# Performance work log

Hardware: AMD Instinct MI355X
Metric: run time of the kernel (lower is better)

Reference implementation:

```python
import jax, jax.numpy as jnp
import numpy as np

# --- constants from config ---
CU, CV, F, BASE = 257.446, 197.718, 387.777, 0.239965
INLIER_THRESHOLD = 0.5
ERROR_TOLERANCE = 0.5   # '3D'
NUM_ITERATIONS = 256
DIM = '3D'
BATCH, NPTS, NSAMP = 64, 16384, 6


def se3_inv(T):
    # T: ...x4x4 SE(3); inverse = [R^T, -R^T t]
    R = T[..., :3, :3]
    t = T[..., :3, 3:4]
    Rt = jnp.swapaxes(R, -1, -2)
    top = jnp.concatenate([Rt, -Rt @ t], axis=-1)
    bottom = jnp.broadcast_to(jnp.array([0.0, 0.0, 0.0, 1.0], T.dtype), top.shape[:-2] + (1, 4))
    return jnp.concatenate([top, bottom], axis=-2)


def weighted_svd_transform(src, trg, w):
    # src, trg: Bx4xS homogeneous points; w: Bx1xS weights. Returns T_trg_src (Bx4x4).
    ps, pt = src[:, :3, :], trg[:, :3, :]
    w_sum = jnp.sum(w, axis=2, keepdims=True)
    cs = jnp.sum(ps * w, axis=2, keepdims=True) / w_sum  # Bx3x1
    ct = jnp.sum(pt * w, axis=2, keepdims=True) / w_sum
    qs, qt = ps - cs, pt - ct
    cov = jnp.einsum('bis,bjs->bij', qt * w, qs)  # Bx3x3
    U, _, Vt = jnp.linalg.svd(cov)
    det = jnp.linalg.det(U @ Vt)
    diag = jnp.stack([jnp.ones_like(det), jnp.ones_like(det), det], axis=-1)  # Bx3
    R = jnp.einsum('bij,bj,bjk->bik', U, diag, Vt)
    t = ct - R @ cs
    top = jnp.concatenate([R, t], axis=2)
    bottom = jnp.broadcast_to(jnp.array([0.0, 0.0, 0.0, 1.0], src.dtype), (src.shape[0], 1, 4))
    return jnp.concatenate([top, bottom], axis=1)


def stereo_project(pts):
    # pts: Bx4xN homogeneous camera-frame points -> Bx4xN stereo image coords (ul, vl, ur, vr)
    M = jnp.array([[F, 0.0, CU, 0.0],
                   [0.0, F, CV, 0.0],
                   [F, 0.0, CU, -F * BASE],
                   [0.0, F, CV, 0.0]], pts.dtype)
    z = pts[:, 2:3, :]
    return jnp.einsum('ij,bjn->bin', M, pts) / z


def setup_inputs() -> dict:
    key = jax.random.key(0)
    ks = jax.random.split(key, 6)
    def homog(k):
        p = jax.random.normal(k, (BATCH, 3, NPTS), jnp.float32) * 5.0
        p = p.at[:, 2, :].set(jnp.abs(p[:, 2, :]) + 1.0)  # positive depth
        return jnp.concatenate([p, jnp.ones((BATCH, 1, NPTS), jnp.float32)], axis=1)
    keypoints_3D_src = homog(ks[0])
    keypoints_3D_trg = homog(ks[1])
    keypoints_2D_trg = jax.random.uniform(ks[2], (BATCH, 2, NPTS), jnp.float32) * 512.0
    valid_pts_src = jax.random.randint(ks[3], (BATCH, 1, NPTS), 0, 2).astype(jnp.int32)
    valid_pts_trg = jax.random.randint(ks[4], (BATCH, 1, NPTS), 0, 2).astype(jnp.int32)
    weights = jax.random.uniform(ks[5], (BATCH, 1, NPTS), jnp.float32, 1e-3, 1.0)
    # vehicle->sensor transform: small rotation about x + translation
    c, s = np.cos(0.1), np.sin(0.1)
    T_s_v = jnp.array([[1, 0, 0, 0.2], [0, c, -s, 0.0], [0, s, c, 1.0], [0, 0, 0, 1]], jnp.float32)
    return {'keypoints_3D_src': keypoints_3D_src, 'keypoints_3D_trg': keypoints_3D_trg,
            'keypoints_2D_trg': keypoints_2D_trg, 'valid_pts_src': valid_pts_src,
            'valid_pts_trg': valid_pts_trg, 'weights': weights, 'T_s_v': T_s_v}


def reference(keypoints_3D_src, keypoints_3D_trg, keypoints_2D_trg,
              valid_pts_src, valid_pts_trg, weights, T_s_v):
    B, _, N = keypoints_3D_src.shape
    pts_src = jax.lax.stop_gradient(keypoints_3D_src)
    pts_trg = jax.lax.stop_gradient(keypoints_3D_trg)
    pts2_trg = jax.lax.stop_gradient(keypoints_2D_trg)
    w = jax.lax.stop_gradient(weights)
    valid = (valid_pts_src[:, 0, :] > 0) & (valid_pts_trg[:, 0, :] > 0)  # BxN
    T_s_v_b = jnp.broadcast_to(T_s_v, (B, 4, 4))
    T_v_s_b = se3_inv(T_s_v_b)

    rand_idx = jax.random.randint(jax.random.key(42), (NUM_ITERATIONS, B, NSAMP), 0, N)

    def body(carry, idx):
        max_inl, inliers = carry
        idx4 = idx[:, None, :]
        s_src = jnp.take_along_axis(pts_src, jnp.broadcast_to(idx4, (B, 4, NSAMP)), axis=2)
        s_trg = jnp.take_along_axis(pts_trg, jnp.broadcast_to(idx4, (B, 4, NSAMP)), axis=2)
        s_w = jnp.take_along_axis(w, idx4, axis=2)
        T_trg_src = weighted_svd_transform(s_src, s_trg, s_w)          # Bx4x4
        T_cam = T_s_v_b @ T_trg_src @ T_v_s_b                          # Bx4x4
        est_3D = jnp.einsum('bij,bjn->bin', T_cam, pts_src)            # Bx4xN
        if DIM == '2D':
            est_2D = stereo_project(est_3D)[:, 0:2, :]
            err = jnp.linalg.norm(pts2_trg - est_2D, axis=1)
        else:
            err = jnp.linalg.norm(pts_trg[:, 0:3, :] - est_3D[:, 0:3, :], axis=1)
        small = (err < ERROR_TOLERANCE) & valid                        # BxN
        num = jnp.sum(small, axis=1).astype(jnp.int32)                 # B
        better = num > max_inl
        inliers = jnp.where(better[:, None], small, inliers)
        max_inl = jnp.where(better, num, max_inl)
        return (max_inl, inliers), None

    init = (jnp.zeros((B,), jnp.int32), jnp.zeros((B, N), bool))
    (_, inliers), _ = jax.lax.scan(body, init, rand_idx)
    return inliers.astype(jnp.float32)
```

## Files before the change

kernel.cpp:

```cpp
#include <hip/hip_runtime.h>
#include <stdint.h>
#include <math.h>

#define NPTS   16384
#define NBATCH 64
#define NITER  256
#define NSAMP  6
#define PPT    8
#define NCHUNK 8
#define ISPLIT 4
#define IPB    (NITER / ISPLIT)

__device__ __forceinline__ uint32_t rotl32(uint32_t v, uint32_t r) {
  return (v << r) | (v >> (32u - r));
}
__device__ __forceinline__ void tf_round(uint32_t& x0, uint32_t& x1, uint32_t r) {
  x0 += x1; x1 = rotl32(x1, r); x1 ^= x0;
}
__device__ void threefry2x32(uint32_t k0, uint32_t k1, uint32_t x0, uint32_t x1,
                             uint32_t& o0, uint32_t& o1) {
  uint32_t ks2 = k0 ^ k1 ^ 0x1BD11BDAu;
  x0 += k0; x1 += k1;
  tf_round(x0,x1,13); tf_round(x0,x1,15); tf_round(x0,x1,26); tf_round(x0,x1,6);
  x0 += k1; x1 += ks2 + 1u;
  tf_round(x0,x1,17); tf_round(x0,x1,29); tf_round(x0,x1,16); tf_round(x0,x1,24);
  x0 += ks2; x1 += k0 + 2u;
  tf_round(x0,x1,13); tf_round(x0,x1,15); tf_round(x0,x1,26); tf_round(x0,x1,6);
  x0 += k0; x1 += k1 + 3u;
  tf_round(x0,x1,17); tf_round(x0,x1,29); tf_round(x0,x1,16); tf_round(x0,x1,24);
  x0 += k1; x1 += ks2 + 4u;
  tf_round(x0,x1,13); tf_round(x0,x1,15); tf_round(x0,x1,26); tf_round(x0,x1,6);
  x0 += ks2; x1 += k0 + 5u;
  o0 = x0; o1 = x1;
}

template<int P, int Q>
__device__ __forceinline__ void jrot(double S[3][3], double V[3][3]) {
  double apq = S[P][Q];
  if (fabs(apq) > 1e-300) {
    double tau = (S[Q][Q] - S[P][P]) / (2.0 * apq);
    double t = copysign(1.0, tau) / (fabs(tau) + sqrt(1.0 + tau * tau));
    double c = 1.0 / sqrt(1.0 + t * t);
    double sn = t * c;
    #pragma unroll
    for (int k = 0; k < 3; ++k) {
      double skp = S[k][P], skq = S[k][Q];
      S[k][P] = c * skp - sn * skq;
      S[k][Q] = sn * skp + c * skq;
    }
    #pragma unroll
    for (int k = 0; k < 3; ++k) {
      double spk = S[P][k], sqk = S[Q][k];
      S[P][k] = c * spk - sn * sqk;
      S[Q][k] = sn * spk + c * sqk;
    }
    #pragma unroll
    for (int k = 0; k < 3; ++k) {
      double vkp = V[k][P], vkq = V[k][Q];
      V[k][P] = c * vkp - sn * vkq;
      V[k][Q] = sn * vkp + c * vkq;
    }
  }
}

__device__ __forceinline__ void swapd(double& a, double& b) { double t=a; a=b; b=t; }

__global__ __launch_bounds__(256) void fit_kernel(
    const float* __restrict__ src, const float* __restrict__ trg,
    const float* __restrict__ wts, const float* __restrict__ Tsv,
    float* __restrict__ models ) {
  const int b = blockIdx.x;
  const int iter = threadIdx.x;

  uint32_t K0, K1;
  threefry2x32(0u, 42u, 0u, 1u, K0, K1);

  const uint32_t base = (uint32_t)((iter * NBATCH + b) * NSAMP);
  int idx[NSAMP];
  #pragma unroll
  for (int s = 0; s < NSAMP; ++s) {
    uint32_t y0, y1;
    threefry2x32(K0, K1, 0u, base + (uint32_t)s, y0, y1);
    idx[s] = (int)((y0 ^ y1) & (uint32_t)(NPTS - 1));
  }

  const float* sb = src + (size_t)b * 4 * NPTS;
  const float* tb = trg + (size_t)b * 4 * NPTS;
  const float* wb = wts + (size_t)b * NPTS;

  float px[NSAMP], py[NSAMP], pz[NSAMP], qx[NSAMP], qy[NSAMP], qz[NSAMP], wv[NSAMP];
  #pragma unroll
  for (int s = 0; s < NSAMP; ++s) {
    int j = idx[s];
    px[s] = sb[j]; py[s] = sb[NPTS + j]; pz[s] = sb[2 * NPTS + j];
    qx[s] = tb[j]; qy[s] = tb[NPTS + j]; qz[s] = tb[2 * NPTS + j];
    wv[s] = wb[j];
  }

  double wsum = 0, csx = 0, csy = 0, csz = 0, ctx = 0, cty = 0, ctz = 0;
  #pragma unroll
  for (int s = 0; s < NSAMP; ++s) {
    double w = (double)wv[s];
    wsum += w;
    csx += (double)px[s] * w; csy += (double)py[s] * w; csz += (double)pz[s] * w;
    ctx += (double)qx[s] * w; cty += (double)qy[s] * w; ctz += (double)qz[s] * w;
  }
  double iw = 1.0 / wsum;
  csx *= iw; csy *= iw; csz *= iw; ctx *= iw; cty *= iw; ctz *= iw;

  double C00=0,C01=0,C02=0,C10=0,C11=0,C12=0,C20=0,C21=0,C22=0;
  #pragma unroll
  for (int s = 0; s < NSAMP; ++s) {
    double w = (double)wv[s];
    double ax = ((double)qx[s]-ctx)*w, ay = ((double)qy[s]-cty)*w, az = ((double)qz[s]-ctz)*w;
    double bx = (double)px[s]-csx, by = (double)py[s]-csy, bz = (double)pz[s]-csz;
    C00 += ax*bx; C01 += ax*by; C02 += ax*bz;
    C10 += ay*bx; C11 += ay*by; C12 += ay*bz;
    C20 += az*bx; C21 += az*by; C22 += az*bz;
  }

  double S[3][3], V[3][3] = {{1,0,0},{0,1,0},{0,0,1}};
  S[0][0] = C00*C00 + C10*C10 + C20*C20;
  S[0][1] = C00*C01 + C10*C11 + C20*C21;
  S[0][2] = C00*C02 + C10*C12 + C20*C22;
  S[1][1] = C01*C01 + C11*C11 + C21*C21;
  S[1][2] = C01*C02 + C11*C12 + C21*C22;
  S[2][2] = C02*C02 + C12*C12 + C22*C22;
  S[1][0] = S[0][1]; S[2][0] = S[0][2]; S[2][1] = S[1][2];
  #pragma unroll 1
  for (int sweep = 0; sweep < 6; ++sweep) {
    jrot<0,1>(S, V); jrot<0,2>(S, V); jrot<1,2>(S, V);
  }

  double l0 = S[0][0], l1 = S[1][1], l2 = S[2][2];
  double v0x=V[0][0], v0y=V[1][0], v0z=V[2][0];
  double v1x=V[0][1], v1y=V[1][1], v1z=V[2][1];
  double v2x=V[0][2], v2y=V[1][2], v2z=V[2][2];
  if (l0 < l1) { swapd(l0,l1); swapd(v0x,v1x); swapd(v0y,v1y); swapd(v0z,v1z); }
  if (l1 < l2) { swapd(l1,l2); swapd(v1x,v2x); swapd(v1y,v2y); swapd(v1z,v2z); }
  if (l0 < l1) { swapd(l0,l1); swapd(v0x,v1x); swapd(v0y,v1y); swapd(v0z,v1z); }

  double u0x = C00*v0x + C01*v0y + C02*v0z;
  double u0y = C10*v0x + C11*v0y + C12*v0z;
  double u0z = C20*v0x + C21*v0y + C22*v0z;
  double n0 = sqrt(u0x*u0x + u0y*u0y + u0z*u0z);
  double r0 = (n0 > 1e-150) ? 1.0 / n0 : 0.0;
  u0x *= r0; u0y *= r0; u0z *= r0;
  double u1x = C00*v1x + C01*v1y + C02*v1z;
  double u1y = C10*v1x + C11*v1y + C12*v1z;
  double u1z = C20*v1x + C21*v1y + C22*v1z;
  double d01 = u1x*u0x + u1y*u0y + u1z*u0z;
  u1x -= d01*u0x; u1y -= d01*u0y; u1z -= d01*u0z;
  double n1 = sqrt(u1x*u1x + u1y*u1y + u1z*u1z);
  double r1 = (n1 > 1e-150) ? 1.0 / n1 : 0.0;
  u1x *= r1; u1y *= r1; u1z *= r1;
  double u2x = u0y*u1z - u0z*u1y;
  double u2y = u0z*u1x - u0x*u1z;
  double u2z = u0x*u1y - u0y*u1x;
  double detV = v0x*(v1y*v2z - v1z*v2y) - v0y*(v1x*v2z - v1z*v2x) + v0z*(v1x*v2y - v1y*v2x);
  double R00 = u0x*v0x + u1x*v1x + detV*u2x*v2x;
  double R01 = u0x*v0y + u1x*v1y + detV*u2x*v2y;
  double R02 = u0x*v0z + u1x*v1z + detV*u2x*v2z;
  double R10 = u0y*v0x + u1y*v1x + detV*u2y*v2x;
  double R11 = u0y*v0y + u1y*v1y + detV*u2y*v2y;
  double R12 = u0y*v0z + u1y*v1z + detV*u2y*v2z;
  double R20 = u0z*v0x + u1z*v1x + detV*u2z*v2x;
  double R21 = u0z*v0y + u1z*v1y + detV*u2z*v2y;
  double R22 = u0z*v0z + u1z*v1z + detV*u2z*v2z;
  double tx = ctx - (R00*csx + R01*csy + R02*csz);
  double ty = cty - (R10*csx + R11*csy + R12*csz);
  double tz = ctz - (R20*csx + R21*csy + R22*csz);

  double A[4][4];
  #pragma unroll
  for (int i = 0; i < 4; ++i)
    #pragma unroll
    for (int j = 0; j < 4; ++j) A[i][j] = (double)Tsv[i*4 + j];
  double Tts[4][4] = {{R00,R01,R02,tx},{R10,R11,R12,ty},{R20,R21,R22,tz},{0,0,0,1}};
  double I[4][4];
  I[0][0]=A[0][0]; I[0][1]=A[1][0]; I[0][2]=A[2][0];
  I[1][0]=A[0][1]; I[1][1]=A[1][1]; I[1][2]=A[2][1];
  I[2][0]=A[0][2]; I[2][1]=A[1][2]; I[2][2]=A[2][2];
  I[0][3] = -(I[0][0]*A[0][3] + I[0][1]*A[1][3] + I[0][2]*A[2][3]);
  I[1][3] = -(I[1][0]*A[0][3] + I[1][1]*A[1][3] + I[1][2]*A[2][3]);
  I[2][3] = -(I[2][0]*A[0][3] + I[2][1]*A[1][3] + I[2][2]*A[2][3]);
  I[3][0]=0; I[3][1]=0; I[3][2]=0; I[3][3]=1;
  double M1[4][4];
  #pragma unroll
  for (int i = 0; i < 4; ++i)
    #pragma unroll
    for (int j = 0; j < 4; ++j)
      M1[i][j] = A[i][0]*Tts[0][j] + A[i][1]*Tts[1][j] + A[i][2]*Tts[2][j] + A[i][3]*Tts[3][j];
  float* mo = models + ((size_t)b * NITER + iter) * 12;
  #pragma unroll
  for (int i = 0; i < 3; ++i)
    #pragma unroll
    for (int j = 0; j < 4; ++j)
      mo[i*4 + j] = (float)(M1[i][0]*I[0][j] + M1[i][1]*I[1][j] + M1[i][2]*I[2][j] + M1[i][3]*I[3][j]);
}

__global__ __launch_bounds__(256) void count_kernel(
    const float* __restrict__ src, const float* __restrict__ trg,
    const int* __restrict__ vs, const int* __restrict__ vt,
    const float* __restrict__ models, int* __restrict__ counts) {
  __shared__ float M[IPB * 12];
  __shared__ int cl[IPB];
  const int b      = blockIdx.x >> 5;
  const int isplit = (blockIdx.x >> 3) & (ISPLIT - 1);
  const int chunk  = blockIdx.x & (NCHUNK - 1);
  const int ibase  = isplit * IPB;

  const float* mb = models + ((size_t)b * NITER + ibase) * 12;
  for (int i = threadIdx.x; i < IPB * 12; i += 256) M[i] = mb[i];
  if (threadIdx.x < IPB) cl[threadIdx.x] = 0;
  __syncthreads();

  const float* sb = src + (size_t)b * 4 * NPTS;
  const float* tb = trg + (size_t)b * 4 * NPTS;
  const int* vsb = vs + (size_t)b * NPTS;
  const int* vtb = vt + (size_t)b * NPTS;
  const int p0 = chunk * (256 * PPT) + threadIdx.x;

  float sx[PPT], sy[PPT], sz[PPT], tx[PPT], ty[PPT], tz[PPT];
  bool vd[PPT];
  #pragma unroll
  for (int k = 0; k < PPT; ++k) {
    int p = p0 + k * 256;
    sx[k] = sb[p]; sy[k] = sb[NPTS + p]; sz[k] = sb[2 * NPTS + p];
    tx[k] = tb[p]; ty[k] = tb[NPTS + p]; tz[k] = tb[2 * NPTS + p];
    vd[k] = (vsb[p] > 0) && (vtb[p] > 0);
  }

  for (int it = 0; it < IPB; ++it) {
    const float* m = &M[it * 12];
    float m00=m[0], m01=m[1], m02=m[2],  m03=m[3];
    float m10=m[4], m11=m[5], m12=m[6],  m13=m[7];
    float m20=m[8], m21=m[9], m22=m[10], m23=m[11];
    int c = 0;
    #pragma unroll
    for (int k = 0; k < PPT; ++k) {
      float ex = fmaf(m00, sx[k], fmaf(m01, sy[k], fmaf(m02, sz[k], m03)));
      float ey = fmaf(m10, sx[k], fmaf(m11, sy[k], fmaf(m12, sz[k], m13)));
      float ez = fmaf(m20, sx[k], fmaf(m21, sy[k], fmaf(m22, sz[k], m23)));
      float dx = tx[k] - ex, dy = ty[k] - ey, dz = tz[k] - ez;
      float e2 = fmaf(dx, dx, fmaf(dy, dy, dz * dz));
      c += (e2 < 0.25f && vd[k]) ? 1 : 0;
    }
    c += __shfl_xor(c, 32); c += __shfl_xor(c, 16); c += __shfl_xor(c, 8);
    c += __shfl_xor(c, 4);  c += __shfl_xor(c, 2);  c += __shfl_xor(c, 1);
    if ((threadIdx.x & 63) == 0) atomicAdd(&cl[it], c);
  }
  __syncthreads();
  if (threadIdx.x < IPB)
    atomicAdd(&counts[(size_t)b * NITER + ibase + threadIdx.x], cl[threadIdx.x]);
}

__global__ __launch_bounds__(64) void argmax_kernel(const int* __restrict__ counts,
                                                    int* __restrict__ win) {
  const int b = blockIdx.x;
  int best = -1;
  for (int it = threadIdx.x; it < NITER; it += 64) {
    int c = counts[b * NITER + it];
    int key = (c << 8) | (NITER - 1 - it);
    best = max(best, key);
  }
  best = max(best, __shfl_xor(best, 32));
  best = max(best, __shfl_xor(best, 16));
  best = max(best, __shfl_xor(best, 8));
  best = max(best, __shfl_xor(best, 4));
  best = max(best, __shfl_xor(best, 2));
  best = max(best, __shfl_xor(best, 1));
  if (threadIdx.x == 0) win[b] = (NITER - 1) - (best & 255);
}

__global__ __launch_bounds__(256) void output_kernel(
    const float* __restrict__ src, const float* __restrict__ trg,
    const int* __restrict__ vs, const int* __restrict__ vt,
    const float* __restrict__ models, const int* __restrict__ win,
    float* __restrict__ out) {
  const int tid = blockIdx.x * 256 + threadIdx.x;
  const int b = tid >> 14;
  const int p = tid & (NPTS - 1);
  const int it = win[b];
  const float* m = models + ((size_t)b * NITER + it) * 12;
  float m00=m[0], m01=m[1], m02=m[2],  m03=m[3];
  float m10=m[4], m11=m[5], m12=m[6],  m13=m[7];
  float m20=m[8], m21=m[9], m22=m[10], m23=m[11];
  const float* sb = src + (size_t)b * 4 * NPTS;
  const float* tb = trg + (size_t)b * 4 * NPTS;
  float sxv = sb[p], syv = sb[NPTS + p], szv = sb[2 * NPTS + p];
  float txv = tb[p], tyv = tb[NPTS + p], tzv = tb[2 * NPTS + p];
  bool v = (vs[(size_t)b * NPTS + p] > 0) && (vt[(size_t)b * NPTS + p] > 0);
  float ex = fmaf(m00, sxv, fmaf(m01, syv, fmaf(m02, szv, m03)));
  float ey = fmaf(m10, sxv, fmaf(m11, syv, fmaf(m12, szv, m13)));
  float ez = fmaf(m20, sxv, fmaf(m21, syv, fmaf(m22, szv, m23)));
  float dx = txv - ex, dy = tyv - ey, dz = tzv - ez;
  float e2 = fmaf(dx, dx, fmaf(dy, dy, dz * dz));
  out[tid] = (e2 < 0.25f && v) ? 1.0f : 0.0f;
}

extern "C" void kernel_launch(void* const* d_in, const int* in_sizes, int n_in,
                              void* d_out, int out_size, void* d_ws, size_t ws_size,
                              hipStream_t stream) {
  (void)in_sizes; (void)n_in; (void)out_size; (void)ws_size;
  const float* src = (const float*)d_in[0];
  const float* trg = (const float*)d_in[1];
  const int*   vs  = (const int*)d_in[3];
  const int*   vt  = (const int*)d_in[4];
  const float* wts = (const float*)d_in[5];
  const float* Tsv = (const float*)d_in[6];
  float* out = (float*)d_out;

  char* ws = (char*)d_ws;
  float* models = (float*)ws;
  int* counts   = (int*)(ws + (size_t)NBATCH * NITER * 12 * 4);
  int* win      = (int*)((char*)counts + (size_t)NBATCH * NITER * 4);

  hipMemsetAsync(counts, 0, (size_t)NBATCH * NITER * sizeof(int), stream);
  fit_kernel<<<NBATCH, NITER, 0, stream>>>(src, trg, wts, Tsv, models);
  count_kernel<<<NBATCH * ISPLIT * NCHUNK, 256, 0, stream>>>(src, trg, vs, vt, models, counts);
  argmax_kernel<<<NBATCH, 64, 0, stream>>>(counts, win);
  output_kernel<<<(NBATCH * NPTS) / 256, 256, 0, stream>>>(src, trg, vs, vt, models, win, out);
}
```

Measured before the change: 229.6 us.

## Fold memset and argmax into neighbouring kernels, split fit blocks, prefetch models

Removes the hipMemsetAsync by having fit_kernel zero the counts, and removes argmax_kernel by recomputing the per-batch argmax inside every output_kernel block. fit_kernel is split into 256 blocks of 64 threads so more CUs take part in the serial SVD work. The count loop software-prefetches the next model's 12 coefficients from shared memory into registers. The goal is fewer launches and less launch-gap overhead, at the cost of redundant argmax reductions in every output block.

```diff
diff --git a/kernel.cpp b/kernel.cpp
--- a/kernel.cpp
+++ b/kernel.cpp
@@ -65,12 +65,15 @@
 
 __device__ __forceinline__ void swapd(double& a, double& b) { double t=a; a=b; b=t; }
 
-__global__ __launch_bounds__(256) void fit_kernel(
+__global__ __launch_bounds__(64) void fit_kernel(
     const float* __restrict__ src, const float* __restrict__ trg,
     const float* __restrict__ wts, const float* __restrict__ Tsv,
-    float* __restrict__ models ) {
-  const int b = blockIdx.x;
-  const int iter = threadIdx.x;
+    float* __restrict__ models ,
+    int* __restrict__ counts ) {
+  const int b = blockIdx.x >> 2;
+  const int iter = ((blockIdx.x & 3) << 6) | threadIdx.x;
+
+  counts[b * NITER + iter] = 0;
 
   uint32_t K0, K1;
   threefry2x32(0u, 42u, 0u, 1u, K0, K1);
@@ -231,11 +234,20 @@
     vd[k] = (vsb[p] > 0) && (vtb[p] > 0);
   }
 
+  float cur[12];
+  #pragma unroll
+  for (int j = 0; j < 12; ++j) cur[j] = M[j];
+
+  #pragma unroll 2
   for (int it = 0; it < IPB; ++it) {
-    const float* m = &M[it * 12];
-    float m00=m[0], m01=m[1], m02=m[2],  m03=m[3];
-    float m10=m[4], m11=m[5], m12=m[6],  m13=m[7];
-    float m20=m[8], m21=m[9], m22=m[10], m23=m[11];
+    const int nit = (it + 1 < IPB) ? it + 1 : it;
+    float nxt[12];
+    #pragma unroll
+    for (int j = 0; j < 12; ++j) nxt[j] = M[nit * 12 + j];
+
+    float m00=cur[0], m01=cur[1], m02=cur[2],  m03=cur[3];
+    float m10=cur[4], m11=cur[5], m12=cur[6],  m13=cur[7];
+    float m20=cur[8], m21=cur[9], m22=cur[10], m23=cur[11];
     int c = 0;
     #pragma unroll
     for (int k = 0; k < PPT; ++k) {
@@ -249,39 +261,40 @@
     c += __shfl_xor(c, 32); c += __shfl_xor(c, 16); c += __shfl_xor(c, 8);
     c += __shfl_xor(c, 4);  c += __shfl_xor(c, 2);  c += __shfl_xor(c, 1);
     if ((threadIdx.x & 63) == 0) atomicAdd(&cl[it], c);
+
+    #pragma unroll
+    for (int j = 0; j < 12; ++j) cur[j] = nxt[j];
   }
   __syncthreads();
   if (threadIdx.x < IPB)
     atomicAdd(&counts[(size_t)b * NITER + ibase + threadIdx.x], cl[threadIdx.x]);
 }
 
-__global__ __launch_bounds__(64) void argmax_kernel(const int* __restrict__ counts,
-                                                    int* __restrict__ win) {
-  const int b = blockIdx.x;
-  int best = -1;
-  for (int it = threadIdx.x; it < NITER; it += 64) {
-    int c = counts[b * NITER + it];
-    int key = (c << 8) | (NITER - 1 - it);
-    best = max(best, key);
-  }
-  best = max(best, __shfl_xor(best, 32));
-  best = max(best, __shfl_xor(best, 16));
-  best = max(best, __shfl_xor(best, 8));
-  best = max(best, __shfl_xor(best, 4));
-  best = max(best, __shfl_xor(best, 2));
-  best = max(best, __shfl_xor(best, 1));
-  if (threadIdx.x == 0) win[b] = (NITER - 1) - (best & 255);
-}
-
 __global__ __launch_bounds__(256) void output_kernel(
     const float* __restrict__ src, const float* __restrict__ trg,
     const int* __restrict__ vs, const int* __restrict__ vt,
-    const float* __restrict__ models, const int* __restrict__ win,
+    const float* __restrict__ models, const int* __restrict__ counts,
     float* __restrict__ out) {
   const int tid = blockIdx.x * 256 + threadIdx.x;
   const int b = tid >> 14;
   const int p = tid & (NPTS - 1);
-  const int it = win[b];
+
+  __shared__ int sbest[4];
+  {
+    int c = counts[b * NITER + threadIdx.x];
+    int key = (c << 8) | (NITER - 1 - threadIdx.x);
+    key = max(key, __shfl_xor(key, 32));
+    key = max(key, __shfl_xor(key, 16));
+    key = max(key, __shfl_xor(key, 8));
+    key = max(key, __shfl_xor(key, 4));
+    key = max(key, __shfl_xor(key, 2));
+    key = max(key, __shfl_xor(key, 1));
+    if ((threadIdx.x & 63) == 0) sbest[threadIdx.x >> 6] = key;
+  }
+  __syncthreads();
+  const int best = max(max(sbest[0], sbest[1]), max(sbest[2], sbest[3]));
+  const int it = (NITER - 1) - (best & 255);
+
   const float* m = models + ((size_t)b * NITER + it) * 12;
   float m00=m[0], m01=m[1], m02=m[2],  m03=m[3];
   float m10=m[4], m11=m[5], m12=m[6],  m13=m[7];
@@ -314,11 +327,8 @@
   char* ws = (char*)d_ws;
   float* models = (float*)ws;
   int* counts   = (int*)(ws + (size_t)NBATCH * NITER * 12 * 4);
-  int* win      = (int*)((char*)counts + (size_t)NBATCH * NITER * 4);
-
-  hipMemsetAsync(counts, 0, (size_t)NBATCH * NITER * sizeof(int), stream);
-  fit_kernel<<<NBATCH, NITER, 0, stream>>>(src, trg, wts, Tsv, models);
+
+  fit_kernel<<<NBATCH * 4, 64, 0, stream>>>(src, trg, wts, Tsv, models, counts);
   count_kernel<<<NBATCH * ISPLIT * NCHUNK, 256, 0, stream>>>(src, trg, vs, vt, models, counts);
-  argmax_kernel<<<NBATCH, 64, 0, stream>>>(counts, win);
-  output_kernel<<<(NBATCH * NPTS) / 256, 256, 0, stream>>>(src, trg, vs, vt, models, win, out);
-}
+  output_kernel<<<(NBATCH * NPTS) / 256, 256, 0, stream>>>(src, trg, vs, vt, models, counts, out);
+}
```

New measurement: 215.1 us. 6.3% less time.
